# Kernel optimization log

Measured on AMD Instinct MI355X. Metric: run time of the kernel, lower is better.

The kernel has to match this reference:

```python
import jax, jax.numpy as jnp
import numpy as np

T, L, N, DR = 8, 8, 500, 32
D = 2 * DR          # dr2 = 64
K = 12              # neighbors per region
S = 2               # number_sp attention layers


def setup_inputs() -> dict:
    key = jax.random.key(0)
    ks = jax.random.split(key, 14)
    inp = {}
    inp["all_data_static"] = jax.random.normal(ks[0], (T, L, N, D), jnp.float32)
    inp["thre_nc"] = jax.random.uniform(ks[1], (T, L, N, 1), jnp.float32)
    inp["all_data_dynamic_now"] = jax.random.uniform(ks[2], (L, N, D), jnp.float32)
    inp["neigh_poi"] = jax.random.randint(ks[3], (N, K), 0, N)
    inp["neigh_road"] = jax.random.randint(ks[4], (N, K), 0, N)
    inp["neigh_record"] = jax.random.randint(ks[5], (N, K), 0, N)
    inp["w1"] = jax.random.normal(ks[6], (2 * D, D), jnp.float32) * 0.05
    inp["wq_all"] = jax.random.normal(ks[7], (2, 3, S, D, D), jnp.float32) * 0.05
    inp["wk_all"] = jax.random.normal(ks[8], (2, 3, S, D, D), jnp.float32) * 0.05
    inp["wd_all"] = jax.random.normal(ks[9], (2, 3, S, D, D), jnp.float32) * 0.05
    inp["wmix_all"] = jax.random.normal(ks[10], (2, 3, D), jnp.float32) * 0.1
    inp["conv_w"] = jax.random.normal(ks[11], (4, 2 * D + 1), jnp.float32) * 0.05
    inp["conv_b"] = jnp.zeros((4,), jnp.float32)
    inp["fin_w"] = jax.random.normal(ks[12], (N, N), jnp.float32) * 0.02
    inp["fin_b"] = jnp.ones((N,), jnp.float32)
    return inp


def _attention(data, neigh, wq, wk, wd):
    # data: (T,L,N,D), neigh: (N,K)
    dn = data[:, :, neigh, :]                                   # (T,L,N,K,D) gather
    q = jnp.einsum('tlnd,de->tlne', data, wq)                   # (T,L,N,D)
    k = jnp.einsum('tlnkd,de->tlnke', dn, wk)                   # (T,L,N,K,D)
    a = jax.nn.softmax(jnp.einsum('tlne,tlnke->tlnk', q, k), -1)
    out = q + jnp.einsum('tlnk,tlnke->tlne', a, k)              # residual on q
    return jax.nn.sigmoid(jnp.einsum('tlnd,de->tlne', out, wd))


def _multiattention(data, neighs, wq, wk, wd, wmix):
    outs = []
    for g in range(3):  # poi, road, record
        x = data
        for s in range(wq.shape[1]):
            x = _attention(x, neighs[g], wq[g, s], wk[g, s], wd[g, s])
        outs.append(x)
    return jax.nn.sigmoid(outs[0] * wmix[0] + outs[1] * wmix[1] + outs[2] * wmix[2])


def reference(all_data_static, thre_nc, all_data_dynamic_now,
              neigh_poi, neigh_road, neigh_record,
              w1, wq_all, wk_all, wd_all, wmix_all,
              conv_w, conv_b, fin_w, fin_b):
    # --- Evolution: gated recurrence over time steps 1..T-1 ---
    def evo_step(now, xs):
        st, th = xs  # (L,N,D), (L,N,1)
        new = jax.nn.sigmoid(jnp.concatenate([now, st], -1) @ w1 * th
                             + now * (1.0 - th))
        return new, (new, new - now)
    now_final, (dyn_rest, diffs) = jax.lax.scan(
        evo_step, all_data_dynamic_now, (all_data_static[1:], thre_nc[1:]))
    all_dyn = jnp.concatenate([all_data_dynamic_now[None], dyn_rest], 0)  # (T,L,N,D)

    neighs = (neigh_poi, neigh_road, neigh_record)
    dyn = _multiattention(all_dyn, neighs, wq_all[0], wk_all[0], wd_all[0], wmix_all[0])
    sta = _multiattention(all_data_static, neighs, wq_all[1], wk_all[1], wd_all[1], wmix_all[1])
    x = jnp.concatenate([dyn, sta], -1)                          # (T,L,N,2D)

    # --- ConvLSTM, kernel (1,1), hidden_dim=1 -> pointwise gated recurrence ---
    h0 = jnp.zeros((x.shape[0], x.shape[2], 1), x.dtype)         # (T,N,1)
    def cell(carry, xt):  # xt: (T,N,2D)
        h, c = carry
        gates = jnp.concatenate([xt, h], -1) @ conv_w.T + conv_b  # (T,N,4)
        i = jax.nn.sigmoid(gates[..., 0:1])
        f = jax.nn.sigmoid(gates[..., 1:2])
        o = jax.nn.sigmoid(gates[..., 2:3])
        g = jnp.tanh(gates[..., 3:4])
        c2 = f * c + i * g
        h2 = o * jnp.tanh(c2)
        return (h2, c2), None
    (h_last, _), _ = jax.lax.scan(cell, (h0, h0), jnp.swapaxes(x, 0, 1))

    out = jax.nn.sigmoid(h_last[..., 0] @ fin_w.T + fin_b)       # (T,N)
    return out, now_final, diffs
```

## Files before the change

### kernel.cpp

```cpp
#include <hip/hip_runtime.h>
#include <math.h>

namespace {
constexpr int kT = 8, kL = 8, kN = 500, kD = 64, kK = 12;
constexpr int kLN  = kL * kN;
constexpr int kTLN = kT * kL * kN;
constexpr int kBUF = kTLN * kD;
constexpr int XS = 68;
}

__device__ __forceinline__ float sigf(float v) { return 1.f / (1.f + __expf(-v)); }

__device__ __forceinline__ void stage_x(const float* __restrict__ src, float* lds,
                                        int row0, int M) {
    int r  = threadIdx.x >> 4;
    int c4 = (threadIdx.x & 15) << 2;
#pragma unroll
    for (int i = 0; i < 4; ++i) {
        int rr  = r + 16 * i;
        int row = row0 + rr;
        row = row < M ? row : M - 1;
        float4 v = *reinterpret_cast<const float4*>(src + (size_t)row * 64 + c4);
        *reinterpret_cast<float4*>(lds + rr * XS + c4) = v;
    }
}

template <int K>
__device__ __forceinline__ void stage_w(const float* __restrict__ w, float* lds) {
    const float4* s = reinterpret_cast<const float4*>(w);
    float4* d = reinterpret_cast<float4*>(lds);
#pragma unroll
    for (int i = 0; i < K / 16; ++i)
        d[threadIdx.x + 256 * i] = s[threadIdx.x + 256 * i];
}

__device__ __forceinline__ void gemm_core(const float* ldsx, const float* ldsw,
                                          int rblk, int cblk, float4 acc[4]) {
#pragma unroll 4
    for (int k = 0; k < 64; k += 4) {
        float4 xv[4], wv[4];
#pragma unroll
        for (int i = 0; i < 4; ++i)
            xv[i] = *reinterpret_cast<const float4*>(ldsx + (4 * rblk + i) * XS + k);
#pragma unroll
        for (int d = 0; d < 4; ++d)
            wv[d] = *reinterpret_cast<const float4*>(ldsw + (k + d) * 64 + 4 * cblk);
#pragma unroll
        for (int i = 0; i < 4; ++i) {
            float xs[4] = {xv[i].x, xv[i].y, xv[i].z, xv[i].w};
#pragma unroll
            for (int d = 0; d < 4; ++d) {
                acc[i].x = fmaf(xs[d], wv[d].x, acc[i].x);
                acc[i].y = fmaf(xs[d], wv[d].y, acc[i].y);
                acc[i].z = fmaf(xs[d], wv[d].z, acc[i].z);
                acc[i].w = fmaf(xs[d], wv[d].w, acc[i].w);
            }
        }
    }
}

__device__ __forceinline__ void gemm_core_gw(const float* ldsx,
                                             const float* __restrict__ gw,
                                             int rblk, int cblk, float4 acc[4]) {
#pragma unroll 4
    for (int k = 0; k < 64; k += 4) {
        float4 xv[4], wv[4];
#pragma unroll
        for (int i = 0; i < 4; ++i)
            xv[i] = *reinterpret_cast<const float4*>(ldsx + (4 * rblk + i) * XS + k);
#pragma unroll
        for (int d = 0; d < 4; ++d)
            wv[d] = *reinterpret_cast<const float4*>(gw + (k + d) * 64 + 4 * cblk);
#pragma unroll
        for (int i = 0; i < 4; ++i) {
            float xs[4] = {xv[i].x, xv[i].y, xv[i].z, xv[i].w};
#pragma unroll
            for (int d = 0; d < 4; ++d) {
                acc[i].x = fmaf(xs[d], wv[d].x, acc[i].x);
                acc[i].y = fmaf(xs[d], wv[d].y, acc[i].y);
                acc[i].z = fmaf(xs[d], wv[d].z, acc[i].z);
                acc[i].w = fmaf(xs[d], wv[d].w, acc[i].w);
            }
        }
    }
}

__device__ __forceinline__ void gemm_core2(const float* ldsx, const float* ldswa,
                                           const float* ldswb, int rblk, int cblk,
                                           float4 acca[4], float4 accb[4]) {
#pragma unroll 4
    for (int k = 0; k < 64; k += 4) {
        float4 xv[4], wa[4], wb[4];
#pragma unroll
        for (int i = 0; i < 4; ++i)
            xv[i] = *reinterpret_cast<const float4*>(ldsx + (4 * rblk + i) * XS + k);
#pragma unroll
        for (int d = 0; d < 4; ++d) {
            wa[d] = *reinterpret_cast<const float4*>(ldswa + (k + d) * 64 + 4 * cblk);
            wb[d] = *reinterpret_cast<const float4*>(ldswb + (k + d) * 64 + 4 * cblk);
        }
#pragma unroll
        for (int i = 0; i < 4; ++i) {
            float xs[4] = {xv[i].x, xv[i].y, xv[i].z, xv[i].w};
#pragma unroll
            for (int d = 0; d < 4; ++d) {
                acca[i].x = fmaf(xs[d], wa[d].x, acca[i].x);
                acca[i].y = fmaf(xs[d], wa[d].y, acca[i].y);
                acca[i].z = fmaf(xs[d], wa[d].z, acca[i].z);
                acca[i].w = fmaf(xs[d], wa[d].w, acca[i].w);
                accb[i].x = fmaf(xs[d], wb[d].x, accb[i].x);
                accb[i].y = fmaf(xs[d], wb[d].y, accb[i].y);
                accb[i].z = fmaf(xs[d], wb[d].z, accb[i].z);
                accb[i].w = fmaf(xs[d], wb[d].w, accb[i].w);
            }
        }
    }
}

__global__ void __launch_bounds__(256) evo_all_kernel(const float* __restrict__ stat,
                                                      const float* __restrict__ thre,
                                                      const float* __restrict__ dyn0,
                                                      float* __restrict__ all_dyn,
                                                      float* __restrict__ diff,
                                                      float* __restrict__ now_final,
                                                      const float* __restrict__ w1) {
    __shared__ float ldsn[64 * XS];
    __shared__ float ldss[64 * XS];
    __shared__ float ldsw[128 * 64];
    int row0 = blockIdx.x * 64;
    stage_x(dyn0, ldsn, row0, kLN);
    stage_w<128>(w1, ldsw);
    int rblk = threadIdx.x >> 4, cblk = threadIdx.x & 15;
    __syncthreads();
#pragma unroll
    for (int i = 0; i < 4; ++i) {
        int row = row0 + 4 * rblk + i;
        if (row < kLN) {
            float4 x0 = *reinterpret_cast<const float4*>(ldsn + (4 * rblk + i) * XS + 4 * cblk);
            *reinterpret_cast<float4*>(all_dyn + (size_t)row * 64 + 4 * cblk) = x0;
        }
    }
#pragma unroll 1
    for (int t = 1; t < kT; ++t) {
        stage_x(stat + (size_t)t * kLN * kD, ldss, row0, kLN);
        __syncthreads();
        float4 acc[4] = {};
        gemm_core(ldsn, ldsw, rblk, cblk, acc);
        gemm_core(ldss, ldsw + 64 * 64, rblk, cblk, acc);
        float4 nv[4];
#pragma unroll
        for (int i = 0; i < 4; ++i) {
            int row = row0 + 4 * rblk + i;
            int rc  = row < kLN ? row : kLN - 1;
            float tt = thre[t * kLN + rc];
            float4 xn = *reinterpret_cast<const float4*>(ldsn + (4 * rblk + i) * XS + 4 * cblk);
            nv[i].x = sigf(acc[i].x * tt + xn.x * (1.f - tt));
            nv[i].y = sigf(acc[i].y * tt + xn.y * (1.f - tt));
            nv[i].z = sigf(acc[i].z * tt + xn.z * (1.f - tt));
            nv[i].w = sigf(acc[i].w * tt + xn.w * (1.f - tt));
            if (row < kLN) {
                float4 df;
                df.x = nv[i].x - xn.x; df.y = nv[i].y - xn.y;
                df.z = nv[i].z - xn.z; df.w = nv[i].w - xn.w;
                *reinterpret_cast<float4*>(all_dyn + ((size_t)t * kLN + row) * 64 + 4 * cblk) = nv[i];
                *reinterpret_cast<float4*>(diff + ((size_t)(t - 1) * kLN + row) * 64 + 4 * cblk) = df;
                if (t == kT - 1)
                    *reinterpret_cast<float4*>(now_final + (size_t)row * 64 + 4 * cblk) = nv[i];
            }
        }
        __syncthreads();
#pragma unroll
        for (int i = 0; i < 4; ++i)
            *reinterpret_cast<float4*>(ldsn + (4 * rblk + i) * XS + 4 * cblk) = nv[i];
    }
}

__global__ void __launch_bounds__(256) gemm_qk(const float* __restrict__ Xdyn,
                                               const float* __restrict__ Xstat,
                                               const float* __restrict__ wq_all,
                                               const float* __restrict__ wk_all,
                                               float* __restrict__ b1,
                                               float* __restrict__ b2, int step) {
    __shared__ float ldsx[64 * XS];
    __shared__ float ldswq[64 * 64];
    __shared__ float ldswk[64 * 64];
    int c = blockIdx.y;
    int m = c / 3;
    float* b1c = b1 + (size_t)c * kBUF;
    float* b2c = b2 + (size_t)c * kBUF;
    const float* X = step ? b1c : (m == 0 ? Xdyn : Xstat);
    size_t woff = (size_t)(c * 2 + step) * kD * kD;
    int row0 = blockIdx.x * 64;
    stage_x(X, ldsx, row0, kTLN);
    stage_w<64>(wq_all + woff, ldswq);
    stage_w<64>(wk_all + woff, ldswk);
    __syncthreads();
    int rblk = threadIdx.x >> 4, cblk = threadIdx.x & 15;
    float4 aq[4] = {}, ak[4] = {};
    gemm_core2(ldsx, ldswq, ldswk, rblk, cblk, aq, ak);
#pragma unroll
    for (int i = 0; i < 4; ++i) {
        size_t row = row0 + 4 * rblk + i;
        *reinterpret_cast<float4*>(b1c + row * 64 + 4 * cblk) = aq[i];
        *reinterpret_cast<float4*>(b2c + row * 64 + 4 * cblk) = ak[i];
    }
}

__global__ void __launch_bounds__(256) scorewd_kernel(float* __restrict__ b1,
                                                      const float* __restrict__ b2,
                                                      const int* __restrict__ npoi,
                                                      const int* __restrict__ nroad,
                                                      const int* __restrict__ nrec,
                                                      const float* __restrict__ wd_all,
                                                      int step) {
    __shared__ float ldsx[64 * XS];
    int p   = blockIdx.y * gridDim.x + blockIdx.x;
    int xcd = p & 7;
    int gid = xcd * 375 + (p >> 3);
    int c    = gid / 500;
    int tile = gid - c * 500;
    int g = c % 3;
    float* b1c = b1 + (size_t)c * kBUF;
    const float* b2c = b2 + (size_t)c * kBUF;
    const int* neigh = (g == 0) ? npoi : (g == 1) ? nroad : nrec;
    const float* gw = wd_all + (size_t)(c * 2 + step) * kD * kD;

    int lane = threadIdx.x & 63;
    int wv   = threadIdx.x >> 6;
    int sub  = lane >> 4;
    int gq   = lane & 15;
    int row0 = tile * 64;
#pragma unroll 1
    for (int pp = 0; pp < 4; ++pp) {
        int lr  = pp * 16 + wv * 4 + sub;
        int row = row0 + lr;
        int n   = row % kN;
        int slab = row - n;
        float4 q = *(reinterpret_cast<const float4*>(b1c) + (size_t)row * 16 + gq);
        const int4* nbp = reinterpret_cast<const int4*>(neigh + n * kK);
        int4 nb0 = nbp[0], nb1 = nbp[1], nb2 = nbp[2];
        int nb[12] = {nb0.x, nb0.y, nb0.z, nb0.w, nb1.x, nb1.y, nb1.z, nb1.w,
                      nb2.x, nb2.y, nb2.z, nb2.w};
        float4 kv[12];
        float sc[12];
#pragma unroll
        for (int j = 0; j < 12; ++j) {
            kv[j] = *(reinterpret_cast<const float4*>(b2c) + (size_t)(slab + nb[j]) * 16 + gq);
            sc[j] = q.x * kv[j].x + q.y * kv[j].y + q.z * kv[j].z + q.w * kv[j].w;
        }
#pragma unroll
        for (int off = 1; off < 16; off <<= 1) {
#pragma unroll
            for (int j = 0; j < 12; ++j) sc[j] += __shfl_xor(sc[j], off, 16);
        }
        float mx = sc[0];
#pragma unroll
        for (int j = 1; j < 12; ++j) mx = fmaxf(mx, sc[j]);
        float ssum = 0.f;
#pragma unroll
        for (int j = 0; j < 12; ++j) { sc[j] = __expf(sc[j] - mx); ssum += sc[j]; }
        float inv = 1.f / ssum;
        float4 o = q;
#pragma unroll
        for (int j = 0; j < 12; ++j) {
            float a = sc[j] * inv;
            o.x = fmaf(a, kv[j].x, o.x);
            o.y = fmaf(a, kv[j].y, o.y);
            o.z = fmaf(a, kv[j].z, o.z);
            o.w = fmaf(a, kv[j].w, o.w);
        }
        *reinterpret_cast<float4*>(ldsx + lr * XS + 4 * gq) = o;
    }
    __syncthreads();
    int rblk = threadIdx.x >> 4, cblk = threadIdx.x & 15;
    float4 acc[4] = {};
    gemm_core_gw(ldsx, gw, rblk, cblk, acc);
#pragma unroll
    for (int i = 0; i < 4; ++i) {
        size_t idx = ((size_t)(row0 + 4 * rblk + i)) * 64 + 4 * cblk;
        float4 y;
        y.x = sigf(acc[i].x); y.y = sigf(acc[i].y);
        y.z = sigf(acc[i].z); y.w = sigf(acc[i].w);
        *reinterpret_cast<float4*>(b1c + idx) = y;
    }
}

__global__ void __launch_bounds__(256) lstm_kernel(const float* __restrict__ b1,
                                                   const float* __restrict__ wmix,
                                                   const float* __restrict__ cw,
                                                   const float* __restrict__ cb,
                                                   float* __restrict__ hlast) {
    int lane = threadIdx.x & 63;
    int wv   = threadIdx.x >> 6;
    int sub  = lane >> 4;
    int fq   = lane & 15;
    int cell = blockIdx.x * 16 + wv * 4 + sub;
    int t = cell / kN, n = cell % kN;
    float wd_[4][4], ws_[4][4], wh[4], bb[4];
#pragma unroll
    for (int gg = 0; gg < 4; ++gg) {
#pragma unroll
        for (int k = 0; k < 4; ++k) {
            wd_[gg][k] = cw[gg * 129 + fq * 4 + k];
            ws_[gg][k] = cw[gg * 129 + 64 + fq * 4 + k];
        }
        wh[gg] = cw[gg * 129 + 128];
        bb[gg] = cb[gg];
    }
    float4 wm[6];
#pragma unroll
    for (int j = 0; j < 6; ++j)
        wm[j] = *reinterpret_cast<const float4*>(wmix + j * 64 + fq * 4);
    float h = 0.f, cc = 0.f;
#pragma unroll 1
    for (int l = 0; l < kL; ++l) {
        size_t row16 = ((size_t)(t * kL + l) * kN + n) * 16 + fq;
        float4 y[6];
#pragma unroll
        for (int j = 0; j < 6; ++j)
            y[j] = *(reinterpret_cast<const float4*>(b1) + (size_t)j * (kBUF / 4) + row16);
        float4 xd, xs;
        xd.x = sigf(y[0].x * wm[0].x + y[1].x * wm[1].x + y[2].x * wm[2].x);
        xd.y = sigf(y[0].y * wm[0].y + y[1].y * wm[1].y + y[2].y * wm[2].y);
        xd.z = sigf(y[0].z * wm[0].z + y[1].z * wm[1].z + y[2].z * wm[2].z);
        xd.w = sigf(y[0].w * wm[0].w + y[1].w * wm[1].w + y[2].w * wm[2].w);
        xs.x = sigf(y[3].x * wm[3].x + y[4].x * wm[4].x + y[5].x * wm[5].x);
        xs.y = sigf(y[3].y * wm[3].y + y[4].y * wm[4].y + y[5].y * wm[5].y);
        xs.z = sigf(y[3].z * wm[3].z + y[4].z * wm[4].z + y[5].z * wm[5].z);
        xs.w = sigf(y[3].w * wm[3].w + y[4].w * wm[4].w + y[5].w * wm[5].w);
        float gsum[4];
#pragma unroll
        for (int gg = 0; gg < 4; ++gg) {
            float v = xd.x * wd_[gg][0] + xd.y * wd_[gg][1]
                    + xd.z * wd_[gg][2] + xd.w * wd_[gg][3];
            v += xs.x * ws_[gg][0] + xs.y * ws_[gg][1]
               + xs.z * ws_[gg][2] + xs.w * ws_[gg][3];
            gsum[gg] = v;
        }
#pragma unroll
        for (int off = 1; off < 16; off <<= 1) {
#pragma unroll
            for (int gg = 0; gg < 4; ++gg) gsum[gg] += __shfl_xor(gsum[gg], off, 16);
        }
        float gi = sigf(gsum[0] + bb[0] + h * wh[0]);
        float gf = sigf(gsum[1] + bb[1] + h * wh[1]);
        float go = sigf(gsum[2] + bb[2] + h * wh[2]);
        float gg_ = tanhf(gsum[3] + bb[3] + h * wh[3]);
        cc = gf * cc + gi * gg_;
        h = go * tanhf(cc);
    }
    if (fq == 0) hlast[cell] = h;
}

__global__ void final_kernel(const float* __restrict__ h, const float* __restrict__ fw,
                             const float* __restrict__ fb, float* __restrict__ out) {
    int wave = threadIdx.x >> 6, lane = threadIdx.x & 63;
    int o = blockIdx.x * 4 + wave;
    int t = o / kN, m = o % kN;
    float acc = 0.f;
    for (int n = lane; n < kN; n += 64)
        acc = fmaf(h[t * kN + n], fw[(size_t)m * kN + n], acc);
#pragma unroll
    for (int off = 32; off > 0; off >>= 1) acc += __shfl_xor(acc, off);
    if (lane == 0) out[o] = sigf(acc + fb[m]);
}

extern "C" void kernel_launch(void* const* d_in, const int* in_sizes, int n_in,
                              void* d_out, int out_size, void* d_ws, size_t ws_size,
                              hipStream_t stream) {
    const float* stat   = (const float*)d_in[0];
    const float* thre   = (const float*)d_in[1];
    const float* dyn0   = (const float*)d_in[2];
    const int*   npoi   = (const int*)d_in[3];
    const int*   nroad  = (const int*)d_in[4];
    const int*   nrec   = (const int*)d_in[5];
    const float* w1     = (const float*)d_in[6];
    const float* wq_all = (const float*)d_in[7];
    const float* wk_all = (const float*)d_in[8];
    const float* wd_all = (const float*)d_in[9];
    const float* wmix   = (const float*)d_in[10];
    const float* conv_w = (const float*)d_in[11];
    const float* conv_b = (const float*)d_in[12];
    const float* fin_w  = (const float*)d_in[13];
    const float* fin_b  = (const float*)d_in[14];

    float* out       = (float*)d_out;
    float* now_final = out + kT * kN;
    float* diffs     = now_final + (size_t)kLN * kD;

    float* ws      = (float*)d_ws;
    float* all_dyn = ws;
    float* b1      = ws + (size_t)kBUF;
    float* b2      = ws + 7 * (size_t)kBUF;
    float* hlast   = ws + 13 * (size_t)kBUF;

    evo_all_kernel<<<(kLN + 63) / 64, 256, 0, stream>>>(stat, thre, dyn0,
                                                        all_dyn, diffs, now_final, w1);

    dim3 agrid(kTLN / 64, 6);
    gemm_qk<<<agrid, 256, 0, stream>>>(all_dyn, stat, wq_all, wk_all, b1, b2, 0);
    scorewd_kernel<<<agrid, 256, 0, stream>>>(b1, b2, npoi, nroad, nrec, wd_all, 0);
    gemm_qk<<<agrid, 256, 0, stream>>>(all_dyn, stat, wq_all, wk_all, b1, b2, 1);
    scorewd_kernel<<<agrid, 256, 0, stream>>>(b1, b2, npoi, nroad, nrec, wd_all, 1);

    lstm_kernel<<<kT * kN / 16, 256, 0, stream>>>(b1, wmix, conv_w, conv_b, hlast);
    final_kernel<<<kT * kN / 4, 256, 0, stream>>>(hlast, fin_w, fin_b, out);
}
```

Baseline: 350.7 us.

## Store attention intermediates in bf16 and read weights directly from global

```diff
diff --git a/kernel.cpp b/kernel.cpp
--- a/kernel.cpp
+++ b/kernel.cpp
@@ -11,6 +11,27 @@
 
 __device__ __forceinline__ float sigf(float v) { return 1.f / (1.f + __expf(-v)); }
 
+__device__ __forceinline__ uint2 pack_bf16x4(float4 v) {
+    auto r = [](float f) {
+        unsigned u = __float_as_uint(f);
+        u += 0x7FFFu + ((u >> 16) & 1u);
+        return u >> 16;
+    };
+    uint2 o;
+    o.x = r(v.x) | (r(v.y) << 16);
+    o.y = r(v.z) | (r(v.w) << 16);
+    return o;
+}
+
+__device__ __forceinline__ float4 unpack_bf16x4(uint2 kk) {
+    float4 f;
+    f.x = __uint_as_float(kk.x << 16);
+    f.y = __uint_as_float(kk.x & 0xFFFF0000u);
+    f.z = __uint_as_float(kk.y << 16);
+    f.w = __uint_as_float(kk.y & 0xFFFF0000u);
+    return f;
+}
+
 __device__ __forceinline__ void stage_x(const float* __restrict__ src, float* lds,
                                         int row0, int M) {
     int r  = threadIdx.x >> 4;
@@ -25,6 +46,18 @@
     }
 }
 
+__device__ __forceinline__ void stage_x_bf16(const unsigned short* __restrict__ src,
+                                             float* lds, int row0) {
+    int r  = threadIdx.x >> 4;
+    int c4 = (threadIdx.x & 15) << 2;
+#pragma unroll
+    for (int i = 0; i < 4; ++i) {
+        int rr = r + 16 * i;
+        uint2 v = *reinterpret_cast<const uint2*>(src + (size_t)(row0 + rr) * 64 + c4);
+        *reinterpret_cast<float4*>(lds + rr * XS + c4) = unpack_bf16x4(v);
+    }
+}
+
 template <int K>
 __device__ __forceinline__ void stage_w(const float* __restrict__ w, float* lds) {
     const float4* s = reinterpret_cast<const float4*>(w);
@@ -34,7 +67,7 @@
         d[threadIdx.x + 256 * i] = s[threadIdx.x + 256 * i];
 }
 
-__device__ __forceinline__ void gemm_core(const float* ldsx, const float* ldsw,
+__device__ __forceinline__ void gemm_core(const float* ldsx, const float* w,
                                           int rblk, int cblk, float4 acc[4]) {
 #pragma unroll 4
     for (int k = 0; k < 64; k += 4) {
@@ -44,7 +77,7 @@
             xv[i] = *reinterpret_cast<const float4*>(ldsx + (4 * rblk + i) * XS + k);
 #pragma unroll
         for (int d = 0; d < 4; ++d)
-            wv[d] = *reinterpret_cast<const float4*>(ldsw + (k + d) * 64 + 4 * cblk);
+            wv[d] = *reinterpret_cast<const float4*>(w + (k + d) * 64 + 4 * cblk);
 #pragma unroll
         for (int i = 0; i < 4; ++i) {
             float xs[4] = {xv[i].x, xv[i].y, xv[i].z, xv[i].w};
@@ -59,61 +92,86 @@
     }
 }
 
-__device__ __forceinline__ void gemm_core_gw(const float* ldsx,
-                                             const float* __restrict__ gw,
-                                             int rblk, int cblk, float4 acc[4]) {
-#pragma unroll 4
-    for (int k = 0; k < 64; k += 4) {
-        float4 xv[4], wv[4];
-#pragma unroll
-        for (int i = 0; i < 4; ++i)
-            xv[i] = *reinterpret_cast<const float4*>(ldsx + (4 * rblk + i) * XS + k);
-#pragma unroll
-        for (int d = 0; d < 4; ++d)
-            wv[d] = *reinterpret_cast<const float4*>(gw + (k + d) * 64 + 4 * cblk);
-#pragma unroll
-        for (int i = 0; i < 4; ++i) {
-            float xs[4] = {xv[i].x, xv[i].y, xv[i].z, xv[i].w};
-#pragma unroll
-            for (int d = 0; d < 4; ++d) {
-                acc[i].x = fmaf(xs[d], wv[d].x, acc[i].x);
-                acc[i].y = fmaf(xs[d], wv[d].y, acc[i].y);
-                acc[i].z = fmaf(xs[d], wv[d].z, acc[i].z);
-                acc[i].w = fmaf(xs[d], wv[d].w, acc[i].w);
-            }
-        }
-    }
-}
-
-__device__ __forceinline__ void gemm_core2(const float* ldsx, const float* ldswa,
-                                           const float* ldswb, int rblk, int cblk,
+__device__ __forceinline__ void gemm_core2(const float* ldsx, const float* wa,
+                                           const float* wb, int rblk, int cblk,
                                            float4 acca[4], float4 accb[4]) {
 #pragma unroll 4
     for (int k = 0; k < 64; k += 4) {
-        float4 xv[4], wa[4], wb[4];
+        float4 xv[4], va[4], vb[4];
 #pragma unroll
         for (int i = 0; i < 4; ++i)
             xv[i] = *reinterpret_cast<const float4*>(ldsx + (4 * rblk + i) * XS + k);
 #pragma unroll
         for (int d = 0; d < 4; ++d) {
-            wa[d] = *reinterpret_cast<const float4*>(ldswa + (k + d) * 64 + 4 * cblk);
-            wb[d] = *reinterpret_cast<const float4*>(ldswb + (k + d) * 64 + 4 * cblk);
+            va[d] = *reinterpret_cast<const float4*>(wa + (k + d) * 64 + 4 * cblk);
+            vb[d] = *reinterpret_cast<const float4*>(wb + (k + d) * 64 + 4 * cblk);
         }
 #pragma unroll
         for (int i = 0; i < 4; ++i) {
             float xs[4] = {xv[i].x, xv[i].y, xv[i].z, xv[i].w};
 #pragma unroll
             for (int d = 0; d < 4; ++d) {
-                acca[i].x = fmaf(xs[d], wa[d].x, acca[i].x);
-                acca[i].y = fmaf(xs[d], wa[d].y, acca[i].y);
-                acca[i].z = fmaf(xs[d], wa[d].z, acca[i].z);
-                acca[i].w = fmaf(xs[d], wa[d].w, acca[i].w);
-                accb[i].x = fmaf(xs[d], wb[d].x, accb[i].x);
-                accb[i].y = fmaf(xs[d], wb[d].y, accb[i].y);
-                accb[i].z = fmaf(xs[d], wb[d].z, accb[i].z);
-                accb[i].w = fmaf(xs[d], wb[d].w, accb[i].w);
+                acca[i].x = fmaf(xs[d], va[d].x, acca[i].x);
+                acca[i].y = fmaf(xs[d], va[d].y, acca[i].y);
+                acca[i].z = fmaf(xs[d], va[d].z, acca[i].z);
+                acca[i].w = fmaf(xs[d], va[d].w, acca[i].w);
+                accb[i].x = fmaf(xs[d], vb[d].x, accb[i].x);
+                accb[i].y = fmaf(xs[d], vb[d].y, accb[i].y);
+                accb[i].z = fmaf(xs[d], vb[d].z, accb[i].z);
+                accb[i].w = fmaf(xs[d], vb[d].w, accb[i].w);
             }
         }
+    }
+}
+
+__device__ __forceinline__ void score_phase(const uint2* __restrict__ Qb,
+                                            const uint2* __restrict__ Kb,
+                                            const int* __restrict__ neigh,
+                                            float* ldsx, int row0) {
+    int lane = threadIdx.x & 63;
+    int wv   = threadIdx.x >> 6;
+    int sub  = lane >> 4;
+    int gq   = lane & 15;
+#pragma unroll 1
+    for (int pp = 0; pp < 4; ++pp) {
+        int lr  = pp * 16 + wv * 4 + sub;
+        int row = row0 + lr;
+        int n   = row % kN;
+        int slab = row - n;
+        float4 q = unpack_bf16x4(Qb[(size_t)row * 16 + gq]);
+        const int4* nbp = reinterpret_cast<const int4*>(neigh + n * kK);
+        int4 nb0 = nbp[0], nb1 = nbp[1], nb2 = nbp[2];
+        int nb[12] = {nb0.x, nb0.y, nb0.z, nb0.w, nb1.x, nb1.y, nb1.z, nb1.w,
+                      nb2.x, nb2.y, nb2.z, nb2.w};
+        float4 kv[12];
+        float sc[12];
+#pragma unroll
+        for (int j = 0; j < 12; ++j) {
+            kv[j] = unpack_bf16x4(Kb[(size_t)(slab + nb[j]) * 16 + gq]);
+            sc[j] = q.x * kv[j].x + q.y * kv[j].y + q.z * kv[j].z + q.w * kv[j].w;
+        }
+#pragma unroll
+        for (int off = 1; off < 16; off <<= 1) {
+#pragma unroll
+            for (int j = 0; j < 12; ++j) sc[j] += __shfl_xor(sc[j], off, 16);
+        }
+        float mx = sc[0];
+#pragma unroll
+        for (int j = 1; j < 12; ++j) mx = fmaxf(mx, sc[j]);
+        float ssum = 0.f;
+#pragma unroll
+        for (int j = 0; j < 12; ++j) { sc[j] = __expf(sc[j] - mx); ssum += sc[j]; }
+        float inv = 1.f / ssum;
+        float4 o = q;
+#pragma unroll
+        for (int j = 0; j < 12; ++j) {
+            float a = sc[j] * inv;
+            o.x = fmaf(a, kv[j].x, o.x);
+            o.y = fmaf(a, kv[j].y, o.y);
+            o.z = fmaf(a, kv[j].z, o.z);
+            o.w = fmaf(a, kv[j].w, o.w);
+        }
+        *reinterpret_cast<float4*>(ldsx + lr * XS + 4 * gq) = o;
     }
 }
 
@@ -179,35 +237,33 @@
                                                const float* __restrict__ Xstat,
                                                const float* __restrict__ wq_all,
                                                const float* __restrict__ wk_all,
-                                               float* __restrict__ b1,
-                                               float* __restrict__ b2, int step) {
+                                               unsigned short* __restrict__ b1,
+                                               unsigned short* __restrict__ b2,
+                                               int step) {
     __shared__ float ldsx[64 * XS];
-    __shared__ float ldswq[64 * 64];
-    __shared__ float ldswk[64 * 64];
     int c = blockIdx.y;
     int m = c / 3;
-    float* b1c = b1 + (size_t)c * kBUF;
-    float* b2c = b2 + (size_t)c * kBUF;
-    const float* X = step ? b1c : (m == 0 ? Xdyn : Xstat);
-    size_t woff = (size_t)(c * 2 + step) * kD * kD;
+    unsigned short* b1c = b1 + (size_t)c * kBUF;
+    unsigned short* kc  = b2 + (size_t)c * kBUF;
+    const float* gwq = wq_all + (size_t)(c * 2 + step) * kD * kD;
+    const float* gwk = wk_all + (size_t)(c * 2 + step) * kD * kD;
     int row0 = blockIdx.x * 64;
-    stage_x(X, ldsx, row0, kTLN);
-    stage_w<64>(wq_all + woff, ldswq);
-    stage_w<64>(wk_all + woff, ldswk);
+    if (step) stage_x_bf16(b1c, ldsx, row0);
+    else      stage_x(m == 0 ? Xdyn : Xstat, ldsx, row0, kTLN);
     __syncthreads();
     int rblk = threadIdx.x >> 4, cblk = threadIdx.x & 15;
     float4 aq[4] = {}, ak[4] = {};
-    gemm_core2(ldsx, ldswq, ldswk, rblk, cblk, aq, ak);
+    gemm_core2(ldsx, gwq, gwk, rblk, cblk, aq, ak);
 #pragma unroll
     for (int i = 0; i < 4; ++i) {
         size_t row = row0 + 4 * rblk + i;
-        *reinterpret_cast<float4*>(b1c + row * 64 + 4 * cblk) = aq[i];
-        *reinterpret_cast<float4*>(b2c + row * 64 + 4 * cblk) = ak[i];
-    }
-}
-
-__global__ void __launch_bounds__(256) scorewd_kernel(float* __restrict__ b1,
-                                                      const float* __restrict__ b2,
+        *reinterpret_cast<uint2*>(b1c + row * 64 + 4 * cblk) = pack_bf16x4(aq[i]);
+        *reinterpret_cast<uint2*>(kc + row * 64 + 4 * cblk)  = pack_bf16x4(ak[i]);
+    }
+}
+
+__global__ void __launch_bounds__(256) scorewd_kernel(unsigned short* __restrict__ b1,
+                                                      const unsigned short* __restrict__ b2,
                                                       const int* __restrict__ npoi,
                                                       const int* __restrict__ nroad,
                                                       const int* __restrict__ nrec,
@@ -220,72 +276,30 @@
     int c    = gid / 500;
     int tile = gid - c * 500;
     int g = c % 3;
-    float* b1c = b1 + (size_t)c * kBUF;
-    const float* b2c = b2 + (size_t)c * kBUF;
+    unsigned short* b1c = b1 + (size_t)c * kBUF;
+    const uint2* Qb = reinterpret_cast<const uint2*>(b1c);
+    const uint2* Kb = reinterpret_cast<const uint2*>(b2 + (size_t)c * kBUF);
     const int* neigh = (g == 0) ? npoi : (g == 1) ? nroad : nrec;
-    const float* gw = wd_all + (size_t)(c * 2 + step) * kD * kD;
-
-    int lane = threadIdx.x & 63;
-    int wv   = threadIdx.x >> 6;
-    int sub  = lane >> 4;
-    int gq   = lane & 15;
+    const float* gwd = wd_all + (size_t)(c * 2 + step) * kD * kD;
     int row0 = tile * 64;
-#pragma unroll 1
-    for (int pp = 0; pp < 4; ++pp) {
-        int lr  = pp * 16 + wv * 4 + sub;
-        int row = row0 + lr;
-        int n   = row % kN;
-        int slab = row - n;
-        float4 q = *(reinterpret_cast<const float4*>(b1c) + (size_t)row * 16 + gq);
-        const int4* nbp = reinterpret_cast<const int4*>(neigh + n * kK);
-        int4 nb0 = nbp[0], nb1 = nbp[1], nb2 = nbp[2];
-        int nb[12] = {nb0.x, nb0.y, nb0.z, nb0.w, nb1.x, nb1.y, nb1.z, nb1.w,
-                      nb2.x, nb2.y, nb2.z, nb2.w};
-        float4 kv[12];
-        float sc[12];
-#pragma unroll
-        for (int j = 0; j < 12; ++j) {
-            kv[j] = *(reinterpret_cast<const float4*>(b2c) + (size_t)(slab + nb[j]) * 16 + gq);
-            sc[j] = q.x * kv[j].x + q.y * kv[j].y + q.z * kv[j].z + q.w * kv[j].w;
-        }
-#pragma unroll
-        for (int off = 1; off < 16; off <<= 1) {
-#pragma unroll
-            for (int j = 0; j < 12; ++j) sc[j] += __shfl_xor(sc[j], off, 16);
-        }
-        float mx = sc[0];
-#pragma unroll
-        for (int j = 1; j < 12; ++j) mx = fmaxf(mx, sc[j]);
-        float ssum = 0.f;
-#pragma unroll
-        for (int j = 0; j < 12; ++j) { sc[j] = __expf(sc[j] - mx); ssum += sc[j]; }
-        float inv = 1.f / ssum;
-        float4 o = q;
-#pragma unroll
-        for (int j = 0; j < 12; ++j) {
-            float a = sc[j] * inv;
-            o.x = fmaf(a, kv[j].x, o.x);
-            o.y = fmaf(a, kv[j].y, o.y);
-            o.z = fmaf(a, kv[j].z, o.z);
-            o.w = fmaf(a, kv[j].w, o.w);
-        }
-        *reinterpret_cast<float4*>(ldsx + lr * XS + 4 * gq) = o;
-    }
+
+    score_phase(Qb, Kb, neigh, ldsx, row0);
     __syncthreads();
+
     int rblk = threadIdx.x >> 4, cblk = threadIdx.x & 15;
     float4 acc[4] = {};
-    gemm_core_gw(ldsx, gw, rblk, cblk, acc);
+    gemm_core(ldsx, gwd, rblk, cblk, acc);
 #pragma unroll
     for (int i = 0; i < 4; ++i) {
-        size_t idx = ((size_t)(row0 + 4 * rblk + i)) * 64 + 4 * cblk;
+        size_t row = row0 + 4 * rblk + i;
         float4 y;
         y.x = sigf(acc[i].x); y.y = sigf(acc[i].y);
         y.z = sigf(acc[i].z); y.w = sigf(acc[i].w);
-        *reinterpret_cast<float4*>(b1c + idx) = y;
-    }
-}
-
-__global__ void __launch_bounds__(256) lstm_kernel(const float* __restrict__ b1,
+        *reinterpret_cast<uint2*>(b1c + row * 64 + 4 * cblk) = pack_bf16x4(y);
+    }
+}
+
+__global__ void __launch_bounds__(256) lstm_kernel(const unsigned short* __restrict__ b1,
                                                    const float* __restrict__ wmix,
                                                    const float* __restrict__ cw,
                                                    const float* __restrict__ cb,
@@ -314,11 +328,11 @@
     float h = 0.f, cc = 0.f;
 #pragma unroll 1
     for (int l = 0; l < kL; ++l) {
-        size_t row16 = ((size_t)(t * kL + l) * kN + n) * 16 + fq;
+        size_t base = ((size_t)(t * kL + l) * kN + n) * 64 + fq * 4;
         float4 y[6];
 #pragma unroll
         for (int j = 0; j < 6; ++j)
-            y[j] = *(reinterpret_cast<const float4*>(b1) + (size_t)j * (kBUF / 4) + row16);
+            y[j] = unpack_bf16x4(*reinterpret_cast<const uint2*>(b1 + (size_t)j * kBUF + base));
         float4 xd, xs;
         xd.x = sigf(y[0].x * wm[0].x + y[1].x * wm[1].x + y[2].x * wm[2].x);
         xd.y = sigf(y[0].y * wm[0].y + y[1].y * wm[1].y + y[2].y * wm[2].y);
@@ -390,9 +404,9 @@
 
     float* ws      = (float*)d_ws;
     float* all_dyn = ws;
-    float* b1      = ws + (size_t)kBUF;
-    float* b2      = ws + 7 * (size_t)kBUF;
-    float* hlast   = ws + 13 * (size_t)kBUF;
+    unsigned short* b1 = (unsigned short*)(ws + (size_t)kBUF);
+    unsigned short* b2 = (unsigned short*)(ws + 4 * (size_t)kBUF);
+    float* hlast   = ws + 7 * (size_t)kBUF;
 
     evo_all_kernel<<<(kLN + 63) / 64, 256, 0, stream>>>(stat, thre, dyn0,
                                                         all_dyn, diffs, now_final, w1);
```

Result: slower. 365.1 us (+4.1%).
